# Kernel tuning notes

Hardware: AMD Instinct MI355X
Metric: run time of the kernel (lower is better)

## Reference

```python
import jax, jax.numpy as jnp
import numpy as np
from jax import lax

NUM_POINTS = 2048  # M, from init_kwargs


def setup_inputs() -> dict:
    key = jax.random.key(0)
    points = jax.random.normal(key, (16, 65536, 3), dtype=jnp.float32)
    return {"points": points}


def farthest_point_sampling(points, num_samples):
    """Iterative D-FPS. points: (B, N, 3) -> indices (B, M) int32."""
    B, N, _ = points.shape
    BIG = jnp.asarray(1e10, points.dtype)

    def step(carry, _):
        min_dist, last_idx = carry          # (B, N), (B,)
        last_pt = jnp.take_along_axis(points, last_idx[:, None, None], axis=1)  # (B,1,3)
        d = jnp.sum((points - last_pt) ** 2, axis=-1)  # (B, N) squared dist to newest centroid
        min_dist = jnp.minimum(min_dist, d)
        nxt = jnp.argmax(min_dist, axis=1).astype(jnp.int32)  # farthest remaining point
        return (min_dist, nxt), nxt

    first = jnp.zeros((B,), dtype=jnp.int32)  # seed with point 0 (standard FPS convention)
    init = (jnp.full((B, N), BIG, points.dtype), first)
    _, rest = lax.scan(step, init, None, length=num_samples - 1)  # (M-1, B)
    indices = jnp.concatenate([first[None, :], rest], axis=0)      # (M, B)
    return indices.T                                                # (B, M)


def reference(points):
    B, N, _ = points.shape
    if N <= NUM_POINTS:
        idx = jnp.broadcast_to(jnp.arange(N, dtype=jnp.int32)[None, :], (B, N))
        return idx
    return farthest_point_sampling(points, NUM_POINTS)
```

## Files before the change

### kernel.cpp

```cpp
#include <hip/hip_runtime.h>


#define N_PTS   65536
#define M_SAMP  2048
#define NT      512
#define BPB     16
#define PTS_BLK (N_PTS / BPB)
#define PPT     (PTS_BLK / NT)
#define NWAVES  (NT / 64)
#define NBATCH  16
#define SLOT_U64 16

typedef unsigned long long u64;

__device__ __forceinline__ u64 ld_agent(const u64* a) {
  return __hip_atomic_load(a, __ATOMIC_RELAXED, __HIP_MEMORY_SCOPE_AGENT);
}
__device__ __forceinline__ void st_agent(u64* a, u64 v) {
  __hip_atomic_store(a, v, __ATOMIC_RELAXED, __HIP_MEMORY_SCOPE_AGENT);
}

__global__ __launch_bounds__(NT, 2)
void fps_multi(const float* __restrict__ pts, int* __restrict__ out,
               u64* __restrict__ ws) {
  const int rank = blockIdx.x;
  const int b    = blockIdx.y;
  const float* __restrict__ p = pts + (size_t)b * (size_t)(N_PTS * 3);
  int* __restrict__ o = out + (size_t)b * M_SAMP;
  const int t = threadIdx.x;
  const int base = rank * PTS_BLK;

  __shared__ float  s_pts[PTS_BLK * 3];
  __shared__ double s_bv[NWAVES];
  __shared__ int    s_bi[NWAVES];
  __shared__ float  s_c[3];

  for (int i = t; i < PTS_BLK * 3; i += NT)
    s_pts[i] = p[base * 3 + i];
  if (rank == 0 && t == 0) o[0] = 0;
  if (t == 0) { s_c[0] = p[0]; s_c[1] = p[1]; s_c[2] = p[2]; }
  __syncthreads();

  double pd[PPT][3];
  double md[PPT];
#pragma unroll
  for (int j = 0; j < PPT; ++j) {
    const int l = t + j * NT;
    pd[j][0] = (double)s_pts[3 * l + 0];
    pd[j][1] = (double)s_pts[3 * l + 1];
    pd[j][2] = (double)s_pts[3 * l + 2];
    md[j] = 1e10;
  }

  for (int m = 1; m < M_SAMP; ++m) {
    const double cx = (double)s_c[0];
    const double cy = (double)s_c[1];
    const double cz = (double)s_c[2];

    double bestv = -1.0;
    int    besti = 0;

#pragma unroll
    for (int j = 0; j < PPT; ++j) {
      const double dx = __dsub_rn(pd[j][0], cx);
      const double dy = __dsub_rn(pd[j][1], cy);
      const double dz = __dsub_rn(pd[j][2], cz);
      const double d  = __dadd_rn(__dadd_rn(__dmul_rn(dx, dx),
                                            __dmul_rn(dy, dy)),
                                  __dmul_rn(dz, dz));
      const double nmd = fmin(md[j], d);
      md[j] = nmd;
      if (nmd > bestv) { bestv = nmd; besti = base + t + j * NT; }
    }

#pragma unroll
    for (int off = 32; off >= 1; off >>= 1) {
      const double ov = __shfl_xor(bestv, off, 64);
      const int    oi = __shfl_xor(besti, off, 64);
      if (ov > bestv || (ov == bestv && oi < besti)) { bestv = ov; besti = oi; }
    }
    if ((t & 63) == 0) { s_bv[t >> 6] = bestv; s_bi[t >> 6] = besti; }
    __syncthreads();

    if (t < 64) {
      if (t < NWAVES) {
        bestv = s_bv[t]; besti = s_bi[t];
#pragma unroll
        for (int off = NWAVES / 2; off >= 1; off >>= 1) {
          const double ov = __shfl_xor(bestv, off, 64);
          const int    oi = __shfl_xor(besti, off, 64);
          if (ov > bestv || (ov == bestv && oi < besti)) { bestv = ov; besti = oi; }
        }
      }
      const u64 mm  = (u64)(unsigned)m;
      const u64 grp = (u64)(((m & 1) * NBATCH + b) * BPB);
      if (t == 0) {
        u64* slot = ws + (grp + rank) * SLOT_U64;
        const int l = besti - base;
        const unsigned xb = __float_as_uint(s_pts[3 * l + 0]);
        const unsigned yb = __float_as_uint(s_pts[3 * l + 1]);
        const unsigned zb = __float_as_uint(s_pts[3 * l + 2]);
        const u64 vb = (u64)__double_as_longlong(bestv);
        const u64 ti = (mm << 16) | (u64)(unsigned)besti;
        st_agent(&slot[0], (vb << 32) | ti);
        st_agent(&slot[1], (vb & 0xFFFFFFFF00000000ull) | ti);
        st_agent(&slot[2], ((u64)xb << 32) | (mm << 16) | (u64)(yb >> 16));
        st_agent(&slot[3], ((u64)(yb & 0xFFFFu) << 48) | ((u64)zb << 16) | mm);
      }
      if (t < BPB) {
        const u64* rs = ws + (grp + t) * SLOT_U64;
        u64 A, B, C, D;
        for (;;) {
          A = ld_agent(rs + 0);
          B = ld_agent(rs + 1);
          C = ld_agent(rs + 2);
          D = ld_agent(rs + 3);
          const bool ok = (((A >> 16) & 0xFFFFull) == mm) &
                          (((B >> 16) & 0xFFFFull) == mm) &
                          (((C >> 16) & 0xFFFFull) == mm) &
                          ((D & 0xFFFFull) == mm);
          if (ok) break;
        }
        double v = __longlong_as_double(
            (long long)((B & 0xFFFFFFFF00000000ull) | (A >> 32)));
        int   i = (int)(A & 0xFFFFull);
        float fx = __uint_as_float((unsigned)(C >> 32));
        float fy = __uint_as_float((unsigned)(((C & 0xFFFFull) << 16) | (D >> 48)));
        float fz = __uint_as_float((unsigned)((D >> 16) & 0xFFFFFFFFull));
        int r = t;
#pragma unroll
        for (int off = BPB / 2; off >= 1; off >>= 1) {
          const double ov = __shfl_xor(v, off, 64);
          const int    oi = __shfl_xor(i, off, 64);
          const int    orr = __shfl_xor(r, off, 64);
          if (ov > v || (ov == v && oi < i)) { v = ov; i = oi; r = orr; }
        }
        fx = __shfl(fx, r, 64);
        fy = __shfl(fy, r, 64);
        fz = __shfl(fz, r, 64);
        if (t == 0) {
          s_c[0] = fx; s_c[1] = fy; s_c[2] = fz;
          if (rank == 0) o[m] = i;
        }
      }
    }
    __syncthreads();
  }
}

extern "C" void kernel_launch(void* const* d_in, const int* in_sizes, int n_in,
                              void* d_out, int out_size, void* d_ws, size_t ws_size,
                              hipStream_t stream) {
  const float* pts = (const float*)d_in[0];
  int* out = (int*)d_out;
  const int B = in_sizes[0] / (N_PTS * 3);
  hipLaunchKernelGGL(fps_multi, dim3(BPB, B), dim3(NT), 0, stream,
                     pts, out, (u64*)d_ws);
}
```

Before: 5.839 ms.

## Remap blocks for XCD locality and add workgroup-scope fast exchange path

Blocks are linearized and remapped so that all 16 ranks of a batch are likely to land on the same XCD under round-robin dispatch. Each block writes its candidate to a second fast slot with workgroup-scope stores. Readers poll those slots with workgroup-scope CAS reads, which the code relies on to be served from the local L2. The fast path is enabled only if a probe at step 1 sees the data, and it falls back to agent-scope polling after a spin limit. The slot stride is also halved. The aim is to cut cross-XCD coherence latency in the per-iteration grid sync, but correctness rests on assumptions about dispatch order and cache behaviour that the code does not enforce.

```diff
diff --git a/kernel.cpp b/kernel.cpp
--- a/kernel.cpp
+++ b/kernel.cpp
@@ -9,7 +9,10 @@
 #define PPT     (PTS_BLK / NT)
 #define NWAVES  (NT / 64)
 #define NBATCH  16
-#define SLOT_U64 16
+#define SLOT_U64 8
+#define FAST_OFF (2 * NBATCH * BPB * SLOT_U64)
+#define PROBE_SPINS 64
+#define FAST_SPINS  1024
 
 typedef unsigned long long u64;
 
@@ -18,13 +21,25 @@
 }
 __device__ __forceinline__ void st_agent(u64* a, u64 v) {
   __hip_atomic_store(a, v, __ATOMIC_RELAXED, __HIP_MEMORY_SCOPE_AGENT);
+}
+__device__ __forceinline__ void st_wg(u64* a, u64 v) {
+  __hip_atomic_store(a, v, __ATOMIC_RELAXED, __HIP_MEMORY_SCOPE_WORKGROUP);
+}
+__device__ __forceinline__ u64 ld_l2(u64* a) {
+  u64 e = 0;
+  __hip_atomic_compare_exchange_strong(a, &e, 0ull, __ATOMIC_RELAXED,
+                                       __ATOMIC_RELAXED,
+                                       __HIP_MEMORY_SCOPE_WORKGROUP);
+  return e;
 }
 
 __global__ __launch_bounds__(NT, 2)
 void fps_multi(const float* __restrict__ pts, int* __restrict__ out,
                u64* __restrict__ ws) {
-  const int rank = blockIdx.x;
-  const int b    = blockIdx.y;
+  const int lid  = blockIdx.x;
+  const int slot = lid >> 3;
+  const int b    = (lid & 7) + ((slot & 1) << 3);
+  const int rank = slot >> 1;
   const float* __restrict__ p = pts + (size_t)b * (size_t)(N_PTS * 3);
   int* __restrict__ o = out + (size_t)b * M_SAMP;
   const int t = threadIdx.x;
@@ -51,6 +66,8 @@
     pd[j][2] = (double)s_pts[3 * l + 2];
     md[j] = 1e10;
   }
+
+  bool fast = false;
 
   for (int m = 1; m < M_SAMP; ++m) {
     const double cx = (double)s_c[0];
@@ -92,34 +109,73 @@
           if (ov > bestv || (ov == bestv && oi < besti)) { bestv = ov; besti = oi; }
         }
       }
-      const u64 mm  = (u64)(unsigned)m;
-      const u64 grp = (u64)(((m & 1) * NBATCH + b) * BPB);
+      const u64 mm = (u64)(unsigned)m;
+      const int pb = ((m & 1) * NBATCH + b) * BPB;
       if (t == 0) {
-        u64* slot = ws + (grp + rank) * SLOT_U64;
         const int l = besti - base;
         const unsigned xb = __float_as_uint(s_pts[3 * l + 0]);
         const unsigned yb = __float_as_uint(s_pts[3 * l + 1]);
         const unsigned zb = __float_as_uint(s_pts[3 * l + 2]);
         const u64 vb = (u64)__double_as_longlong(bestv);
         const u64 ti = (mm << 16) | (u64)(unsigned)besti;
-        st_agent(&slot[0], (vb << 32) | ti);
-        st_agent(&slot[1], (vb & 0xFFFFFFFF00000000ull) | ti);
-        st_agent(&slot[2], ((u64)xb << 32) | (mm << 16) | (u64)(yb >> 16));
-        st_agent(&slot[3], ((u64)(yb & 0xFFFFu) << 48) | ((u64)zb << 16) | mm);
+        const u64 Aw = (vb << 32) | ti;
+        const u64 Bw = (vb & 0xFFFFFFFF00000000ull) | ti;
+        const u64 Cw = ((u64)xb << 32) | (mm << 16) | (u64)(yb >> 16);
+        const u64 Dw = ((u64)(yb & 0xFFFFu) << 48) | ((u64)zb << 16) | mm;
+        u64* fs = ws + FAST_OFF + (size_t)(pb + rank) * SLOT_U64;
+        st_wg(fs + 0, Aw);
+        st_wg(fs + 1, Bw);
+        st_wg(fs + 2, Cw);
+        st_wg(fs + 3, Dw);
+        u64* s = ws + (size_t)(pb + rank) * SLOT_U64;
+        st_agent(&s[0], Aw);
+        st_agent(&s[1], Bw);
+        st_agent(&s[2], Cw);
+        st_agent(&s[3], Dw);
       }
       if (t < BPB) {
-        const u64* rs = ws + (grp + t) * SLOT_U64;
         u64 A, B, C, D;
-        for (;;) {
-          A = ld_agent(rs + 0);
-          B = ld_agent(rs + 1);
-          C = ld_agent(rs + 2);
-          D = ld_agent(rs + 3);
-          const bool ok = (((A >> 16) & 0xFFFFull) == mm) &
-                          (((B >> 16) & 0xFFFFull) == mm) &
-                          (((C >> 16) & 0xFFFFull) == mm) &
-                          ((D & 0xFFFFull) == mm);
-          if (ok) break;
+        bool got = false;
+        u64* fs = ws + FAST_OFF + (size_t)(pb + t) * SLOT_U64;
+        if (fast) {
+          for (int sp = 0; sp < FAST_SPINS; ++sp) {
+            A = ld_l2(fs + 0);
+            B = ld_l2(fs + 1);
+            C = ld_l2(fs + 2);
+            D = ld_l2(fs + 3);
+            const bool ok = (((A >> 16) & 0xFFFFull) == mm) &
+                            (((B >> 16) & 0xFFFFull) == mm) &
+                            (((C >> 16) & 0xFFFFull) == mm) &
+                            ((D & 0xFFFFull) == mm);
+            if (ok) { got = true; break; }
+          }
+          if (!got) fast = false;
+        }
+        if (!got) {
+          const u64* rs = ws + (size_t)(pb + t) * SLOT_U64;
+          for (;;) {
+            A = ld_agent(rs + 0);
+            B = ld_agent(rs + 1);
+            C = ld_agent(rs + 2);
+            D = ld_agent(rs + 3);
+            const bool ok = (((A >> 16) & 0xFFFFull) == mm) &
+                            (((B >> 16) & 0xFFFFull) == mm) &
+                            (((C >> 16) & 0xFFFFull) == mm) &
+                            ((D & 0xFFFFull) == mm);
+            if (ok) break;
+          }
+          if (m == 1) {
+            for (int sp = 0; sp < PROBE_SPINS && !fast; ++sp) {
+              const u64 a2 = ld_l2(fs + 0);
+              const u64 b2 = ld_l2(fs + 1);
+              const u64 c2 = ld_l2(fs + 2);
+              const u64 d2 = ld_l2(fs + 3);
+              fast = (((a2 >> 16) & 0xFFFFull) == mm) &
+                     (((b2 >> 16) & 0xFFFFull) == mm) &
+                     (((c2 >> 16) & 0xFFFFull) == mm) &
+                     ((d2 & 0xFFFFull) == mm);
+            }
+          }
         }
         double v = __longlong_as_double(
             (long long)((B & 0xFFFFFFFF00000000ull) | (A >> 32)));
@@ -154,6 +210,6 @@
   const float* pts = (const float*)d_in[0];
   int* out = (int*)d_out;
   const int B = in_sizes[0] / (N_PTS * 3);
-  hipLaunchKernelGGL(fps_multi, dim3(BPB, B), dim3(NT), 0, stream,
+  hipLaunchKernelGGL(fps_multi, dim3(BPB * B), dim3(NT), 0, stream,
                      pts, out, (u64*)d_ws);
 }
```

Result: slower. 10.45 ms (+78.9%).

## Publish per-wave candidates globally and replace block barriers with LDS flag polling

Applied to the files above, without the earlier changes.

Each wave now publishes its local best candidate, with point coordinates and a step tag, straight to global workspace slots. Wave 0 of every block gathers all 128 wave candidates for its batch and reduces them with shuffles, then broadcasts the chosen centroid to the other waves through tagged LDS words instead of __syncthreads. This drops the intra-block shared-memory reduction and both block barriers per step. In exchange it adds eight times more global slots to poll and spin loops on LDS, and it keeps the old kernel as a fallback when the workspace is too small.

```diff
diff --git a/kernel.cpp b/kernel.cpp
--- a/kernel.cpp
+++ b/kernel.cpp
@@ -9,7 +9,6 @@
 #define PPT     (PTS_BLK / NT)
 #define NWAVES  (NT / 64)
 #define NBATCH  16
-#define SLOT_U64 16
 
 typedef unsigned long long u64;
 
@@ -19,26 +18,36 @@
 __device__ __forceinline__ void st_agent(u64* a, u64 v) {
   __hip_atomic_store(a, v, __ATOMIC_RELAXED, __HIP_MEMORY_SCOPE_AGENT);
 }
+__device__ __forceinline__ u64 ld_lds(const u64* a) {
+  return __hip_atomic_load(a, __ATOMIC_RELAXED, __HIP_MEMORY_SCOPE_WORKGROUP);
+}
+__device__ __forceinline__ void st_lds(u64* a, u64 v) {
+  __hip_atomic_store(a, v, __ATOMIC_RELAXED, __HIP_MEMORY_SCOPE_WORKGROUP);
+}
+
+#define WSLOT_U64 4
+#define SLOTS_PER_BATCH (BPB * NWAVES)
+#define WREGION_U64 (NBATCH * SLOTS_PER_BATCH * WSLOT_U64)
+#define WS_NEED ((size_t)(2 * WREGION_U64) * 8)
 
 __global__ __launch_bounds__(NT, 2)
-void fps_multi(const float* __restrict__ pts, int* __restrict__ out,
-               u64* __restrict__ ws) {
+void fps_wavepub(const float* __restrict__ pts, int* __restrict__ out,
+                 u64* __restrict__ ws) {
   const int rank = blockIdx.x;
   const int b    = blockIdx.y;
   const float* __restrict__ p = pts + (size_t)b * (size_t)(N_PTS * 3);
   int* __restrict__ o = out + (size_t)b * M_SAMP;
   const int t = threadIdx.x;
+  const int w = t >> 6, lane = t & 63;
   const int base = rank * PTS_BLK;
 
-  __shared__ float  s_pts[PTS_BLK * 3];
-  __shared__ double s_bv[NWAVES];
-  __shared__ int    s_bi[NWAVES];
-  __shared__ float  s_c[3];
+  __shared__ float s_pts[PTS_BLK * 3];
+  __shared__ u64   sL[2][3];
 
   for (int i = t; i < PTS_BLK * 3; i += NT)
     s_pts[i] = p[base * 3 + i];
   if (rank == 0 && t == 0) o[0] = 0;
-  if (t == 0) { s_c[0] = p[0]; s_c[1] = p[1]; s_c[2] = p[2]; }
+  if (t < 6) sL[t / 3][t % 3] = 0xAAAAAAAAAAAAAAAAull;
   __syncthreads();
 
   double pd[PPT][3];
@@ -52,11 +61,9 @@
     md[j] = 1e10;
   }
 
+  double cx = (double)p[0], cy = (double)p[1], cz = (double)p[2];
+
   for (int m = 1; m < M_SAMP; ++m) {
-    const double cx = (double)s_c[0];
-    const double cy = (double)s_c[1];
-    const double cz = (double)s_c[2];
-
     double bestv = -1.0;
     int    besti = 0;
 
@@ -79,6 +86,158 @@
       const int    oi = __shfl_xor(besti, off, 64);
       if (ov > bestv || (ov == bestv && oi < besti)) { bestv = ov; besti = oi; }
     }
+
+    const u64 mm  = (u64)(unsigned)m;
+    const int par = m & 1;
+    u64* reg = ws + (size_t)par * WREGION_U64 +
+               (size_t)b * (SLOTS_PER_BATCH * WSLOT_U64);
+
+    if (lane == 0) {
+      const int l = besti - base;
+      const unsigned xb = __float_as_uint(s_pts[3 * l + 0]);
+      const unsigned yb = __float_as_uint(s_pts[3 * l + 1]);
+      const unsigned zb = __float_as_uint(s_pts[3 * l + 2]);
+      const u64 vb = (u64)__double_as_longlong(bestv);
+      const u64 ti = (mm << 16) | (u64)(unsigned)besti;
+      u64* s = reg + (size_t)(rank * NWAVES + w) * WSLOT_U64;
+      st_agent(s + 0, (vb << 32) | ti);
+      st_agent(s + 1, (vb & 0xFFFFFFFF00000000ull) | ti);
+      st_agent(s + 2, ((u64)xb << 32) | (mm << 16) | (u64)(yb >> 16));
+      st_agent(s + 3, ((u64)(yb & 0xFFFFu) << 48) | ((u64)zb << 16) | mm);
+    }
+
+    if (w == 0) {
+      const u64* r0 = reg + (size_t)(2 * lane) * WSLOT_U64;
+      const u64* r1 = reg + (size_t)(2 * lane + 1) * WSLOT_U64;
+      u64 A0, B0, C0, D0, A1, B1, C1, D1;
+      for (;;) {
+        A0 = ld_agent(r0 + 0); B0 = ld_agent(r0 + 1);
+        C0 = ld_agent(r0 + 2); D0 = ld_agent(r0 + 3);
+        A1 = ld_agent(r1 + 0); B1 = ld_agent(r1 + 1);
+        C1 = ld_agent(r1 + 2); D1 = ld_agent(r1 + 3);
+        const bool ok = (((A0 >> 16) & 0xFFFFull) == mm) &
+                        (((B0 >> 16) & 0xFFFFull) == mm) &
+                        (((C0 >> 16) & 0xFFFFull) == mm) &
+                        ((D0 & 0xFFFFull) == mm) &
+                        (((A1 >> 16) & 0xFFFFull) == mm) &
+                        (((B1 >> 16) & 0xFFFFull) == mm) &
+                        (((C1 >> 16) & 0xFFFFull) == mm) &
+                        ((D1 & 0xFFFFull) == mm);
+        if (ok) break;
+      }
+      const double v0 = __longlong_as_double(
+          (long long)((B0 & 0xFFFFFFFF00000000ull) | (A0 >> 32)));
+      const double v1 = __longlong_as_double(
+          (long long)((B1 & 0xFFFFFFFF00000000ull) | (A1 >> 32)));
+      const int i0 = (int)(A0 & 0xFFFFull);
+      const int i1 = (int)(A1 & 0xFFFFull);
+      const bool take1 = (v1 > v0) || (v1 == v0 && i1 < i0);
+      double v  = take1 ? v1 : v0;
+      int    ii = take1 ? i1 : i0;
+      int    src = lane | ((take1 ? 1 : 0) << 6);
+#pragma unroll
+      for (int off = 32; off >= 1; off >>= 1) {
+        const double ov = __shfl_xor(v, off, 64);
+        const int    oi = __shfl_xor(ii, off, 64);
+        const int    os = __shfl_xor(src, off, 64);
+        if (ov > v || (ov == v && oi < ii)) { v = ov; ii = oi; src = os; }
+      }
+      const int own  = src & 63;
+      const int half = src >> 6;
+      unsigned sx = half ? (unsigned)(C1 >> 32) : (unsigned)(C0 >> 32);
+      unsigned sy = half ? (unsigned)(((C1 & 0xFFFFull) << 16) | (D1 >> 48))
+                         : (unsigned)(((C0 & 0xFFFFull) << 16) | (D0 >> 48));
+      unsigned sz = half ? (unsigned)((D1 >> 16) & 0xFFFFFFFFull)
+                         : (unsigned)((D0 >> 16) & 0xFFFFFFFFull);
+      const unsigned cxb = (unsigned)__shfl((int)sx, own, 64);
+      const unsigned cyb = (unsigned)__shfl((int)sy, own, 64);
+      const unsigned czb = (unsigned)__shfl((int)sz, own, 64);
+      if (lane == 0) {
+        st_lds(&sL[par][0], ((u64)cxb << 32) | mm);
+        st_lds(&sL[par][1], ((u64)cyb << 32) | mm);
+        st_lds(&sL[par][2], ((u64)czb << 32) | mm);
+        if (rank == 0) o[m] = ii;
+      }
+      cx = (double)__uint_as_float(cxb);
+      cy = (double)__uint_as_float(cyb);
+      cz = (double)__uint_as_float(czb);
+    } else {
+      u64 l0, l1, l2;
+      for (;;) {
+        l0 = ld_lds(&sL[par][0]);
+        l1 = ld_lds(&sL[par][1]);
+        l2 = ld_lds(&sL[par][2]);
+        const bool ok = ((l0 & 0xFFFFull) == mm) &
+                        ((l1 & 0xFFFFull) == mm) &
+                        ((l2 & 0xFFFFull) == mm);
+        if (ok) break;
+      }
+      cx = (double)__uint_as_float((unsigned)(l0 >> 32));
+      cy = (double)__uint_as_float((unsigned)(l1 >> 32));
+      cz = (double)__uint_as_float((unsigned)(l2 >> 32));
+    }
+  }
+}
+
+#define BSLOT_U64 16
+
+__global__ __launch_bounds__(NT, 2)
+void fps_multi(const float* __restrict__ pts, int* __restrict__ out,
+               u64* __restrict__ ws) {
+  const int rank = blockIdx.x;
+  const int b    = blockIdx.y;
+  const float* __restrict__ p = pts + (size_t)b * (size_t)(N_PTS * 3);
+  int* __restrict__ o = out + (size_t)b * M_SAMP;
+  const int t = threadIdx.x;
+  const int base = rank * PTS_BLK;
+
+  __shared__ float  s_pts[PTS_BLK * 3];
+  __shared__ double s_bv[NWAVES];
+  __shared__ int    s_bi[NWAVES];
+  __shared__ float  s_c[3];
+
+  for (int i = t; i < PTS_BLK * 3; i += NT)
+    s_pts[i] = p[base * 3 + i];
+  if (rank == 0 && t == 0) o[0] = 0;
+  if (t == 0) { s_c[0] = p[0]; s_c[1] = p[1]; s_c[2] = p[2]; }
+  __syncthreads();
+
+  double pd[PPT][3];
+  double md[PPT];
+#pragma unroll
+  for (int j = 0; j < PPT; ++j) {
+    const int l = t + j * NT;
+    pd[j][0] = (double)s_pts[3 * l + 0];
+    pd[j][1] = (double)s_pts[3 * l + 1];
+    pd[j][2] = (double)s_pts[3 * l + 2];
+    md[j] = 1e10;
+  }
+
+  for (int m = 1; m < M_SAMP; ++m) {
+    const double cx = (double)s_c[0];
+    const double cy = (double)s_c[1];
+    const double cz = (double)s_c[2];
+
+    double bestv = -1.0;
+    int    besti = 0;
+#pragma unroll
+    for (int j = 0; j < PPT; ++j) {
+      const double dx = __dsub_rn(pd[j][0], cx);
+      const double dy = __dsub_rn(pd[j][1], cy);
+      const double dz = __dsub_rn(pd[j][2], cz);
+      const double d  = __dadd_rn(__dadd_rn(__dmul_rn(dx, dx),
+                                            __dmul_rn(dy, dy)),
+                                  __dmul_rn(dz, dz));
+      const double nmd = fmin(md[j], d);
+      md[j] = nmd;
+      if (nmd > bestv) { bestv = nmd; besti = base + t + j * NT; }
+    }
+#pragma unroll
+    for (int off = 32; off >= 1; off >>= 1) {
+      const double ov = __shfl_xor(bestv, off, 64);
+      const int    oi = __shfl_xor(besti, off, 64);
+      if (ov > bestv || (ov == bestv && oi < besti)) { bestv = ov; besti = oi; }
+    }
     if ((t & 63) == 0) { s_bv[t >> 6] = bestv; s_bi[t >> 6] = besti; }
     __syncthreads();
 
@@ -95,7 +254,7 @@
       const u64 mm  = (u64)(unsigned)m;
       const u64 grp = (u64)(((m & 1) * NBATCH + b) * BPB);
       if (t == 0) {
-        u64* slot = ws + (grp + rank) * SLOT_U64;
+        u64* slot = ws + (grp + rank) * BSLOT_U64;
         const int l = besti - base;
         const unsigned xb = __float_as_uint(s_pts[3 * l + 0]);
         const unsigned yb = __float_as_uint(s_pts[3 * l + 1]);
@@ -108,7 +267,7 @@
         st_agent(&slot[3], ((u64)(yb & 0xFFFFu) << 48) | ((u64)zb << 16) | mm);
       }
       if (t < BPB) {
-        const u64* rs = ws + (grp + t) * SLOT_U64;
+        const u64* rs = ws + (grp + t) * BSLOT_U64;
         u64 A, B, C, D;
         for (;;) {
           A = ld_agent(rs + 0);
@@ -154,6 +313,11 @@
   const float* pts = (const float*)d_in[0];
   int* out = (int*)d_out;
   const int B = in_sizes[0] / (N_PTS * 3);
-  hipLaunchKernelGGL(fps_multi, dim3(BPB, B), dim3(NT), 0, stream,
-                     pts, out, (u64*)d_ws);
-}
+  if (ws_size >= WS_NEED) {
+    hipLaunchKernelGGL(fps_wavepub, dim3(BPB, B), dim3(NT), 0, stream,
+                       pts, out, (u64*)d_ws);
+  } else {
+    hipLaunchKernelGGL(fps_multi, dim3(BPB, B), dim3(NT), 0, stream,
+                       pts, out, (u64*)d_ws);
+  }
+}
```

Measured after the change: 12.86 ms. 120% more time.

## Split publish and poll across waves, replace second barrier with LDS mailbox

Applied to the files above, without the earlier changes.

Wave 1 now does the block-level reduction and publishes the block's candidate to global workspace, while wave 0 polls the other blocks' slots in parallel. Wave 0 broadcasts the new centroid through a parity-double-buffered LDS mailbox tagged with the iteration number; the other waves spin on that mailbox instead of waiting at a second __syncthreads. Output indices are buffered in shared memory and written once at the end. The aim is to shorten the per-iteration critical path of the cross-block handoff. In exchange, seven waves busy-poll LDS, and correctness now depends on the tag protocol and on relaxed workgroup-scope atomics.

```diff
diff --git a/kernel.cpp b/kernel.cpp
--- a/kernel.cpp
+++ b/kernel.cpp
@@ -19,26 +19,34 @@
 __device__ __forceinline__ void st_agent(u64* a, u64 v) {
   __hip_atomic_store(a, v, __ATOMIC_RELAXED, __HIP_MEMORY_SCOPE_AGENT);
 }
+__device__ __forceinline__ u64 ld_lds(const u64* a) {
+  return __hip_atomic_load(a, __ATOMIC_RELAXED, __HIP_MEMORY_SCOPE_WORKGROUP);
+}
+__device__ __forceinline__ void st_lds(u64* a, u64 v) {
+  __hip_atomic_store(a, v, __ATOMIC_RELAXED, __HIP_MEMORY_SCOPE_WORKGROUP);
+}
 
 __global__ __launch_bounds__(NT, 2)
-void fps_multi(const float* __restrict__ pts, int* __restrict__ out,
+void fps_split(const float* __restrict__ pts, int* __restrict__ out,
                u64* __restrict__ ws) {
   const int rank = blockIdx.x;
   const int b    = blockIdx.y;
   const float* __restrict__ p = pts + (size_t)b * (size_t)(N_PTS * 3);
   int* __restrict__ o = out + (size_t)b * M_SAMP;
   const int t = threadIdx.x;
+  const int w = t >> 6, lane = t & 63;
   const int base = rank * PTS_BLK;
 
   __shared__ float  s_pts[PTS_BLK * 3];
   __shared__ double s_bv[NWAVES];
   __shared__ int    s_bi[NWAVES];
-  __shared__ float  s_c[3];
+  __shared__ u64    sMB[2][3];
+  __shared__ int    s_out[M_SAMP];
 
   for (int i = t; i < PTS_BLK * 3; i += NT)
     s_pts[i] = p[base * 3 + i];
-  if (rank == 0 && t == 0) o[0] = 0;
-  if (t == 0) { s_c[0] = p[0]; s_c[1] = p[1]; s_c[2] = p[2]; }
+  if (t == 0) s_out[0] = 0;
+  if (t < 6) sMB[t / 3][t % 3] = 0xAAAAAAAAAAAAAAAAull;
   __syncthreads();
 
   double pd[PPT][3];
@@ -52,11 +60,9 @@
     md[j] = 1e10;
   }
 
+  double cx = (double)p[0], cy = (double)p[1], cz = (double)p[2];
+
   for (int m = 1; m < M_SAMP; ++m) {
-    const double cx = (double)s_c[0];
-    const double cy = (double)s_c[1];
-    const double cz = (double)s_c[2];
-
     double bestv = -1.0;
     int    besti = 0;
 
@@ -79,36 +85,43 @@
       const int    oi = __shfl_xor(besti, off, 64);
       if (ov > bestv || (ov == bestv && oi < besti)) { bestv = ov; besti = oi; }
     }
-    if ((t & 63) == 0) { s_bv[t >> 6] = bestv; s_bi[t >> 6] = besti; }
+    if (lane == 0) { s_bv[w] = bestv; s_bi[w] = besti; }
     __syncthreads();
 
-    if (t < 64) {
-      if (t < NWAVES) {
-        bestv = s_bv[t]; besti = s_bi[t];
-#pragma unroll
-        for (int off = NWAVES / 2; off >= 1; off >>= 1) {
-          const double ov = __shfl_xor(bestv, off, 64);
-          const int    oi = __shfl_xor(besti, off, 64);
-          if (ov > bestv || (ov == bestv && oi < besti)) { bestv = ov; besti = oi; }
-        }
-      }
-      const u64 mm  = (u64)(unsigned)m;
-      const u64 grp = (u64)(((m & 1) * NBATCH + b) * BPB);
-      if (t == 0) {
+    const u64 mm  = (u64)(unsigned)m;
+    const int par = m & 1;
+    const u64 grp = (u64)((par * NBATCH + b) * BPB);
+
+    if (w == 1) {
+      double rv = -1.0;
+      int    ri = 0x7FFFFFFF;
+      if (lane < NWAVES) { rv = s_bv[lane]; ri = s_bi[lane]; }
+#pragma unroll
+      for (int off = NWAVES / 2; off >= 1; off >>= 1) {
+        const double ov = __shfl_xor(rv, off, 64);
+        const int    oi = __shfl_xor(ri, off, 64);
+        if (ov > rv || (ov == rv && oi < ri)) { rv = ov; ri = oi; }
+      }
+      if (lane == 0) {
         u64* slot = ws + (grp + rank) * SLOT_U64;
-        const int l = besti - base;
+        const int l = ri - base;
         const unsigned xb = __float_as_uint(s_pts[3 * l + 0]);
         const unsigned yb = __float_as_uint(s_pts[3 * l + 1]);
         const unsigned zb = __float_as_uint(s_pts[3 * l + 2]);
-        const u64 vb = (u64)__double_as_longlong(bestv);
-        const u64 ti = (mm << 16) | (u64)(unsigned)besti;
+        const u64 vb = (u64)__double_as_longlong(rv);
+        const u64 ti = (mm << 16) | (u64)(unsigned)ri;
         st_agent(&slot[0], (vb << 32) | ti);
         st_agent(&slot[1], (vb & 0xFFFFFFFF00000000ull) | ti);
         st_agent(&slot[2], ((u64)xb << 32) | (mm << 16) | (u64)(yb >> 16));
         st_agent(&slot[3], ((u64)(yb & 0xFFFFu) << 48) | ((u64)zb << 16) | mm);
       }
-      if (t < BPB) {
-        const u64* rs = ws + (grp + t) * SLOT_U64;
+    }
+
+    if (w == 0) {
+      unsigned cxb = 0, cyb = 0, czb = 0;
+      int ii = 0;
+      if (lane < BPB) {
+        const u64* rs = ws + (grp + lane) * SLOT_U64;
         u64 A, B, C, D;
         for (;;) {
           A = ld_agent(rs + 0);
@@ -123,29 +136,58 @@
         }
         double v = __longlong_as_double(
             (long long)((B & 0xFFFFFFFF00000000ull) | (A >> 32)));
-        int   i = (int)(A & 0xFFFFull);
+        ii = (int)(A & 0xFFFFull);
         float fx = __uint_as_float((unsigned)(C >> 32));
         float fy = __uint_as_float((unsigned)(((C & 0xFFFFull) << 16) | (D >> 48)));
         float fz = __uint_as_float((unsigned)((D >> 16) & 0xFFFFFFFFull));
-        int r = t;
+        int r = lane;
 #pragma unroll
         for (int off = BPB / 2; off >= 1; off >>= 1) {
           const double ov = __shfl_xor(v, off, 64);
-          const int    oi = __shfl_xor(i, off, 64);
+          const int    oi = __shfl_xor(ii, off, 64);
           const int    orr = __shfl_xor(r, off, 64);
-          if (ov > v || (ov == v && oi < i)) { v = ov; i = oi; r = orr; }
+          if (ov > v || (ov == v && oi < ii)) { v = ov; ii = oi; r = orr; }
         }
         fx = __shfl(fx, r, 64);
         fy = __shfl(fy, r, 64);
         fz = __shfl(fz, r, 64);
-        if (t == 0) {
-          s_c[0] = fx; s_c[1] = fy; s_c[2] = fz;
-          if (rank == 0) o[m] = i;
-        }
-      }
-    }
-    __syncthreads();
+        cxb = __float_as_uint(fx);
+        cyb = __float_as_uint(fy);
+        czb = __float_as_uint(fz);
+      }
+      cxb = (unsigned)__shfl((int)cxb, 0, 64);
+      cyb = (unsigned)__shfl((int)cyb, 0, 64);
+      czb = (unsigned)__shfl((int)czb, 0, 64);
+      ii  = __shfl(ii, 0, 64);
+      if (lane == 0) {
+        if (rank == 0) s_out[m] = ii;
+        st_lds(&sMB[par][0], ((u64)cxb << 32) | mm);
+        st_lds(&sMB[par][1], ((u64)cyb << 32) | mm);
+        st_lds(&sMB[par][2], ((u64)czb << 32) | mm);
+      }
+      cx = (double)__uint_as_float(cxb);
+      cy = (double)__uint_as_float(cyb);
+      cz = (double)__uint_as_float(czb);
+    } else {
+      u64 l0, l1, l2;
+      for (;;) {
+        l0 = ld_lds(&sMB[par][0]);
+        l1 = ld_lds(&sMB[par][1]);
+        l2 = ld_lds(&sMB[par][2]);
+        const bool ok = ((l0 & 0xFFFFull) == mm) &
+                        ((l1 & 0xFFFFull) == mm) &
+                        ((l2 & 0xFFFFull) == mm);
+        if (ok) break;
+      }
+      cx = (double)__uint_as_float((unsigned)(l0 >> 32));
+      cy = (double)__uint_as_float((unsigned)(l1 >> 32));
+      cz = (double)__uint_as_float((unsigned)(l2 >> 32));
+    }
   }
+
+  __syncthreads();
+  if (rank == 0)
+    for (int i = t; i < M_SAMP; i += NT) o[i] = s_out[i];
 }
 
 extern "C" void kernel_launch(void* const* d_in, const int* in_sizes, int n_in,
@@ -154,6 +196,6 @@
   const float* pts = (const float*)d_in[0];
   int* out = (int*)d_out;
   const int B = in_sizes[0] / (N_PTS * 3);
-  hipLaunchKernelGGL(fps_multi, dim3(BPB, B), dim3(NT), 0, stream,
+  hipLaunchKernelGGL(fps_split, dim3(BPB, B), dim3(NT), 0, stream,
                      pts, out, (u64*)d_ws);
 }
```

Result: slower. 7.168 ms (+22.8%).
